# Performance work log

Hardware: AMD Instinct MI355X
Metric: run time of the kernel (lower is better)

## Reference

```python
import jax, jax.numpy as jnp
import numpy as np

B, N, D = 2, 2048, 1024
H, DH = 16, 64
DEPTH = 4
FF = 4
EPS = 1e-3  # keras LayerNormalization default epsilon
SCALE = DH ** -0.5


def setup_inputs() -> dict:
    key = jax.random.key(0)
    ks = jax.random.split(key, 8)
    s = 0.02
    inner = H * DH
    return {
        "x": jax.random.normal(ks[0], (B, N, D), jnp.float32),
        "mask": jnp.ones((B, N), jnp.bool_),
        "ln1_g": jnp.ones((DEPTH, D), jnp.float32),
        "ln1_b": jnp.zeros((DEPTH, D), jnp.float32),
        "Wqkv": jax.random.normal(ks[1], (DEPTH, D, 3 * inner), jnp.float32) * s,
        "Wout": jax.random.normal(ks[2], (DEPTH, inner, D), jnp.float32) * s,
        "bout": jnp.zeros((DEPTH, D), jnp.float32),
        "ln2_g": jnp.ones((DEPTH, D), jnp.float32),
        "ln2_b": jnp.zeros((DEPTH, D), jnp.float32),
        "W1": jax.random.normal(ks[3], (DEPTH, D, 2 * FF * D), jnp.float32) * s,
        "b1": jnp.zeros((DEPTH, 2 * FF * D), jnp.float32),
        "W2": jax.random.normal(ks[4], (DEPTH, FF * D, D), jnp.float32) * s,
        "b2": jnp.zeros((DEPTH, D), jnp.float32),
    }


def _layernorm(x, g, b):
    mu = jnp.mean(x, axis=-1, keepdims=True)
    var = jnp.mean(jnp.square(x - mu), axis=-1, keepdims=True)
    return (x - mu) * jax.lax.rsqrt(var + EPS) * g + b


def _attention(x, mask, Wqkv, Wout, bout):
    b, n, _ = x.shape
    qkv = x @ Wqkv  # [b, n, 3*h*dh]
    q, k, v = jnp.split(qkv, 3, axis=-1)
    split_heads = lambda t: t.reshape(b, n, H, DH).transpose(0, 2, 1, 3)  # b h n d
    q, k, v = split_heads(q), split_heads(k), split_heads(v)
    dots = jnp.einsum("bhid,bhjd->bhij", q, k) * SCALE
    neg = -jnp.finfo(dots.dtype).max
    # padding mask: keep (i valid) & (j valid)
    pm = mask[:, None, :, None] & mask[:, None, None, :]
    dots = jnp.where(pm, dots, neg)
    # causal mask: strict upper triangle masked out (triu with k=1)
    causal = jnp.triu(jnp.ones((n, n), jnp.bool_), k=1)
    dots = jnp.where(causal, neg, dots)
    attn = jax.nn.softmax(dots, axis=-1)
    out = jnp.einsum("bhij,bhjd->bhid", attn, v)
    out = out.transpose(0, 2, 1, 3).reshape(b, n, H * DH)
    return out @ Wout + bout


def _feedforward(x, W1, b1, W2, b2):
    h = x @ W1 + b1
    a, gates = jnp.split(h, 2, axis=-1)
    h = a * jax.nn.gelu(gates, approximate=False)  # GEGLU, tf.nn.gelu exact
    return h @ W2 + b2


def reference(x, mask, ln1_g, ln1_b, Wqkv, Wout, bout, ln2_g, ln2_b, W1, b1, W2, b2):
    for l in range(DEPTH):
        x = x + _attention(_layernorm(x, ln1_g[l], ln1_b[l]), mask, Wqkv[l], Wout[l], bout[l])
        x = x + _feedforward(_layernorm(x, ln2_g[l], ln2_b[l]), W1[l], b1[l], W2[l], b2[l])
    return x
```

## Files before the change

### kernel.cpp

```cpp
#include <hip/hip_runtime.h>


typedef float f32x4 __attribute__((ext_vector_type(4)));
typedef __bf16 bf16x8 __attribute__((ext_vector_type(8)));
typedef unsigned short u16;
typedef unsigned int u32;

#define SCALE2 0.18033688011112042f
#define LN_EPS 1e-3f
#define DEFER_THR 8.0f

__device__ __forceinline__ float fexp2(float x) { return __builtin_amdgcn_exp2f(x); }

__device__ __forceinline__ u16 f2bf(float f) {
  u32 u = __float_as_uint(f);
  u += 0x7fffu + ((u >> 16) & 1u);
  return (u16)(u >> 16);
}

__device__ __forceinline__ void stage16(void* lds_wave_base, const void* gsrc) {
  __builtin_amdgcn_global_load_lds((__attribute__((address_space(1))) void*)gsrc,
                                   (__attribute__((address_space(3))) void*)lds_wave_base,
                                   16, 0, 0);
}

__global__ void wtrans_kernel(const float* __restrict__ W, u16* __restrict__ WT,
                              int K, int N, int permMode) {
  __shared__ float tile[32][33];
  const int n0 = blockIdx.x * 32, k0 = blockIdx.y * 32;
  const float* Wl = W + (size_t)blockIdx.z * K * N;
  u16* WTl = WT + (size_t)blockIdx.z * K * N;
  const int tx = threadIdx.x, ty = threadIdx.y;
#pragma unroll
  for (int i = 0; i < 4; ++i)
    tile[ty + i * 8][tx] = Wl[(size_t)(k0 + ty + i * 8) * N + n0 + tx];
  __syncthreads();
#pragma unroll
  for (int i = 0; i < 4; ++i) {
    const int n = n0 + ty + i * 8;
    int orow;
    if (permMode) {
      orow = (n < 4096) ? (((n >> 4) << 5) + (n & 15))
                        : ((((n - 4096) >> 4) << 5) + 16 + (n & 15));
    } else {
      orow = n;
    }
    WTl[(size_t)orow * K + k0 + tx] = f2bf(tile[tx][ty + i * 8]);
  }
}

__global__ void vtrans_kernel(const u16* __restrict__ qkv, u16* __restrict__ Vt) {
  __shared__ u16 tile[32][33];
  const int t0 = blockIdx.x * 32, d0 = blockIdx.y * 32, bh = blockIdx.z;
  const int b = bh >> 4, h = bh & 15;
  const int tx = threadIdx.x, ty = threadIdx.y;
#pragma unroll
  for (int i = 0; i < 4; ++i)
    tile[ty + i * 8][tx] =
        qkv[((size_t)(b * 2048 + t0 + ty + i * 8)) * 3072 + 2048 + h * 64 + d0 + tx];
  __syncthreads();
#pragma unroll
  for (int i = 0; i < 4; ++i)
    Vt[((size_t)bh * 64 + d0 + ty + i * 8) * 2048 + t0 + tx] = tile[tx][ty + i * 8];
}

__global__ __launch_bounds__(256, 4)
void ln_kernel(const float* __restrict__ x, const float* __restrict__ g,
               const float* __restrict__ b, u16* __restrict__ y) {
  const int row = blockIdx.x, tid = threadIdx.x;
  const float4 v = ((const float4*)(x + (size_t)row * 1024))[tid];
  float s = v.x + v.y + v.z + v.w;
  float s2 = v.x * v.x + v.y * v.y + v.z * v.z + v.w * v.w;
#pragma unroll
  for (int off = 32; off > 0; off >>= 1) {
    s += __shfl_down(s, off);
    s2 += __shfl_down(s2, off);
  }
  __shared__ float ps[8];
  __shared__ float stats[2];
  const int wv = tid >> 6, lane = tid & 63;
  if (lane == 0) { ps[wv] = s; ps[wv + 4] = s2; }
  __syncthreads();
  if (tid == 0) {
    const float S = ps[0] + ps[1] + ps[2] + ps[3];
    const float S2 = ps[4] + ps[5] + ps[6] + ps[7];
    const float mu = S * (1.0f / 1024.0f);
    const float var = S2 * (1.0f / 1024.0f) - mu * mu;
    stats[0] = mu;
    stats[1] = rsqrtf(var + LN_EPS);
  }
  __syncthreads();
  const float mu = stats[0], rs = stats[1];
  const float4 gg = ((const float4*)g)[tid];
  const float4 bb = ((const float4*)b)[tid];
  ushort4 ov;
  ov.x = f2bf((v.x - mu) * rs * gg.x + bb.x);
  ov.y = f2bf((v.y - mu) * rs * gg.y + bb.y);
  ov.z = f2bf((v.z - mu) * rs * gg.z + bb.z);
  ov.w = f2bf((v.w - mu) * rs * gg.w + bb.w);
  ((ushort4*)(y + (size_t)row * 1024))[tid] = ov;
}

template <int EPI, int BM, int BN, int WM, int WN>
__global__ __launch_bounds__(WM * WN * 64, 2)
void gemm2(const u16* __restrict__ A, const u16* __restrict__ B,
           float* __restrict__ resid, const float* __restrict__ bias,
           u16* __restrict__ out, int M, int N, int K) {
  constexpr int NTHR = WM * WN * 64;
  constexpr int MT = BM / WM / 16;
  constexpr int NT = BN / WN / 16;
  constexpr int QM = MT / 4;
  __shared__ __align__(16) u16 lds[2][(BM + BN) * 64];

  const int tid = threadIdx.x;
  const int wv = tid >> 6, lane = tid & 63;
  const int lr = lane & 15, lg = lane >> 4;
  const int wmi = wv / WN, wni = wv % WN;

  const int nwg = (int)(gridDim.x * gridDim.y);
  int id = (int)(blockIdx.y * gridDim.x + blockIdx.x);
  id = (id & 7) * (nwg >> 3) + (id >> 3);
  const int m0 = (id / (int)gridDim.x) * BM, n0 = (id % (int)gridDim.x) * BN;

  auto stage = [&](int bsel, int k0) {
    u16* dstA = &lds[bsel][0];
    u16* dstB = &lds[bsel][BM * 64];
#pragma unroll
    for (int rnd = 0; rnd < (BM * 128) / (NTHR * 16); ++rnd) {
      const int base = rnd * (NTHR * 16) + wv * 1024;
      const int off = base + lane * 16;
      const int row = off >> 7;
      const int k2 = (off & 127) ^ ((row & 7) << 4);
      stage16((char*)dstA + base, A + (size_t)(m0 + row) * K + k0 + (k2 >> 1));
    }
#pragma unroll
    for (int rnd = 0; rnd < (BN * 128) / (NTHR * 16); ++rnd) {
      const int base = rnd * (NTHR * 16) + wv * 1024;
      const int off = base + lane * 16;
      const int row = off >> 7;
      const int k2 = (off & 127) ^ ((row & 7) << 4);
      stage16((char*)dstB + base, B + (size_t)(n0 + row) * K + k0 + (k2 >> 1));
    }
  };

  f32x4 acc[MT][NT] = {};

  const int nT = K >> 6;
  stage(0, 0);
  stage(1, 64);
  asm volatile("s_waitcnt vmcnt(8)\n\ts_barrier" ::: "memory");

  for (int t = 0; t < nT; ++t) {
    const u16* As = &lds[t & 1][0];
    const u16* Bs = &lds[t & 1][BM * 64];
#pragma unroll
    for (int ks = 0; ks < 2; ++ks) {
      bf16x8 bfr[NT];
#pragma unroll
      for (int nt = 0; nt < NT; ++nt) {
        const int row = wni * (BN / WN) + nt * 16 + lr;
        bfr[nt] = *(const bf16x8*)((const char*)Bs + row * 128 +
                                   ((ks * 64 + lg * 16) ^ ((lr & 7) << 4)));
      }
#pragma unroll
      for (int qm = 0; qm < QM; ++qm) {
        bf16x8 afr[4];
#pragma unroll
        for (int i = 0; i < 4; ++i) {
          const int row = wmi * (BM / WM) + (qm * 4 + i) * 16 + lr;
          afr[i] = *(const bf16x8*)((const char*)As + row * 128 +
                                    ((ks * 64 + lg * 16) ^ ((lr & 7) << 4)));
        }
        __builtin_amdgcn_s_setprio(1);
#pragma unroll
        for (int i = 0; i < 4; ++i)
#pragma unroll
          for (int nt = 0; nt < NT; ++nt)
            acc[qm * 4 + i][nt] = __builtin_amdgcn_mfma_f32_16x16x32_bf16(
                afr[i], bfr[nt], acc[qm * 4 + i][nt], 0, 0, 0);
        __builtin_amdgcn_s_setprio(0);
      }
    }
    __syncthreads();
    if (t + 2 < nT) stage(t & 1, (t + 2) * 64);
    asm volatile("s_barrier" ::: "memory");
  }

  const int RB0 = wmi * (BM / WM), CB0 = wni * (BN / WN);
  if (EPI == 0) {
#pragma unroll
    for (int mt = 0; mt < MT; ++mt)
#pragma unroll
      for (int nt = 0; nt < NT; ++nt) {
        const int n = n0 + CB0 + nt * 16 + lr;
#pragma unroll
        for (int r = 0; r < 4; ++r) {
          const int m = m0 + RB0 + mt * 16 + lg * 4 + r;
          out[(size_t)m * N + n] = f2bf(acc[mt][nt][r]);
        }
      }
  } else if (EPI == 1) {
    float bs[NT];
#pragma unroll
    for (int nt = 0; nt < NT; ++nt) bs[nt] = bias[n0 + CB0 + nt * 16 + lr];
#pragma unroll
    for (int mt = 0; mt < MT; ++mt)
#pragma unroll
      for (int nt = 0; nt < NT; ++nt) {
        const int n = n0 + CB0 + nt * 16 + lr;
#pragma unroll
        for (int r = 0; r < 4; ++r) {
          const int m = m0 + RB0 + mt * 16 + lg * 4 + r;
          resid[(size_t)m * N + n] += acc[mt][nt][r] + bs[nt];
        }
      }
  } else {
#pragma unroll
    for (int pt = 0; pt < NT / 2; ++pt) {
      const int colA = ((n0 + CB0 + pt * 32) >> 5) * 16 + lr;
      const float ba = bias[colA];
      const float bg = bias[4096 + colA];
#pragma unroll
      for (int mt = 0; mt < MT; ++mt)
#pragma unroll
        for (int r = 0; r < 4; ++r) {
          const int m = m0 + RB0 + mt * 16 + lg * 4 + r;
          const float a = acc[mt][2 * pt][r] + ba;
          const float g = acc[mt][2 * pt + 1][r] + bg;
          const float gl = 0.5f * g * (1.0f + erff(g * 0.70710678118654752f));
          out[(size_t)m * 4096 + colA] = f2bf(a * gl);
        }
    }
  }
}

__global__ __launch_bounds__(512, 4)
void attn_kernel(const u16* __restrict__ qkv, const u16* __restrict__ Vt,
                 u16* __restrict__ attnout) {
  __shared__ __align__(16) u16 KV[2][2][64 * 64];
  __shared__ __align__(16) u16 Ps[8][16 * 64];

  const int tid = threadIdx.x;
  const int wv = tid >> 6, lane = tid & 63;
  const int lr = lane & 15, lg = lane >> 4;
  const int lin = (int)(blockIdx.y * gridDim.x + blockIdx.x);
  const int xcd = lin & 7, j = lin >> 3;
  const int bh = xcd * 4 + (j >> 4);
  const int pr = j & 15;
  const int b = bh >> 4, h = bh & 15;
  const size_t tokbase = (size_t)b * 2048;
  const int qhi = 31 - pr;
  const int qt = (wv < 4) ? qhi : pr;
  const int ws = wv & 3;
  const int qg = qt * 64 + ws * 16 + lr;

  bf16x8 qf[2];
#pragma unroll
  for (int ks = 0; ks < 2; ++ks)
    qf[ks] = *(const bf16x8*)(qkv + (tokbase + qt * 64 + ws * 16 + lr) * 3072 +
                              h * 64 + ks * 32 + lg * 8);

  f32x4 o[4] = {};
  float m = -1e30f, lp = 0.f;

  const u16* kg_base = qkv + tokbase * 3072 + 1024 + h * 64;
  const u16* vg_base = Vt + (size_t)bh * 64 * 2048;

  const int soff = tid * 16;
  const int srow = soff >> 7;
  const int scol = (soff & 127) ^ ((srow & 7) << 4);
  auto stage = [&](int bsel, int kt2) {
    stage16((char*)&KV[bsel][0][0] + wv * 1024,
            kg_base + (size_t)(kt2 * 64 + srow) * 3072 + (scol >> 1));
    stage16((char*)&KV[bsel][1][0] + wv * 1024,
            vg_base + (size_t)srow * 2048 + kt2 * 64 + (scol >> 1));
  };

  stage(0, 0);
  stage(1, 1);
  asm volatile("s_waitcnt vmcnt(2)\n\ts_barrier" ::: "memory");

  for (int kt = 0; kt <= qhi; ++kt) {
    if (kt <= qt) {
      const char* Ks = (const char*)&KV[kt & 1][0][0];
      const char* Vs = (const char*)&KV[kt & 1][1][0];

      f32x4 s[4] = {};
#pragma unroll
      for (int ks = 0; ks < 2; ++ks)
#pragma unroll
        for (int nt = 0; nt < 4; ++nt) {
          const int row = nt * 16 + lr;
          const bf16x8 kf = *(const bf16x8*)(Ks + row * 128 +
                                             ((ks * 64 + lg * 16) ^ ((lr & 7) << 4)));
          s[nt] = __builtin_amdgcn_mfma_f32_16x16x32_bf16(kf, qf[ks], s[nt], 0, 0, 0);
        }

      float pmax = -1e30f;
      const bool diag = (kt == qt);
#pragma unroll
      for (int nt = 0; nt < 4; ++nt)
#pragma unroll
        for (int r = 0; r < 4; ++r) {
          float v = s[nt][r] * SCALE2;
          if (diag) {
            const int kg = kt * 64 + nt * 16 + lg * 4 + r;
            v = (kg <= qg) ? v : -1e30f;
          }
          s[nt][r] = v;
          pmax = fmaxf(pmax, v);
        }

      if (!__all(pmax - m <= DEFER_THR)) {
        float mx = fmaxf(pmax, __shfl_xor(pmax, 16));
        mx = fmaxf(mx, __shfl_xor(mx, 32));
        const float mn = fmaxf(m, mx);
        const float alpha = fexp2(m - mn);
        m = mn;
        lp *= alpha;
#pragma unroll
        for (int r = 0; r < 4; ++r) {
          const float ar = __shfl(alpha, lg * 4 + r);
#pragma unroll
          for (int dt = 0; dt < 4; ++dt) o[dt][r] *= ar;
        }
      }

#pragma unroll
      for (int nt = 0; nt < 4; ++nt) {
        const float p0 = fexp2(s[nt][0] - m), p1 = fexp2(s[nt][1] - m);
        const float p2 = fexp2(s[nt][2] - m), p3 = fexp2(s[nt][3] - m);
        lp += (p0 + p1) + (p2 + p3);
        uint2 w;
        w.x = (u32)f2bf(p0) | ((u32)f2bf(p1) << 16);
        w.y = (u32)f2bf(p2) | ((u32)f2bf(p3) << 16);
        *(uint2*)((char*)&Ps[wv][0] + lr * 128 + ((nt * 32 + lg * 8) ^ ((lr & 7) << 4))) = w;
      }

      bf16x8 pf[2];
#pragma unroll
      for (int ks = 0; ks < 2; ++ks) {
        const int jp = (ks * 4 + lg) ^ (lr & 7);
        pf[ks] = *(const bf16x8*)(&Ps[wv][0] + lr * 64 + jp * 8);
      }
#pragma unroll
      for (int ks = 0; ks < 2; ++ks)
#pragma unroll
        for (int dt = 0; dt < 4; ++dt) {
          const int row = dt * 16 + lr;
          const bf16x8 vf = *(const bf16x8*)(Vs + row * 128 +
                                             ((ks * 64 + lg * 16) ^ ((lr & 7) << 4)));
          o[dt] = __builtin_amdgcn_mfma_f32_16x16x32_bf16(pf[ks], vf, o[dt], 0, 0, 0);
        }
    }

    __syncthreads();
    if (kt + 2 <= qhi) stage(kt & 1, kt + 2);
    asm volatile("s_barrier" ::: "memory");
  }

  float lsum = lp + __shfl_xor(lp, 16);
  lsum += __shfl_xor(lsum, 32);
#pragma unroll
  for (int r = 0; r < 4; ++r) {
    const float ld = __shfl(lsum, lg * 4 + r);
    const int tok = qt * 64 + ws * 16 + lg * 4 + r;
#pragma unroll
    for (int dt = 0; dt < 4; ++dt)
      attnout[(tokbase + tok) * 1024 + h * 64 + dt * 16 + lr] = f2bf(o[dt][r] / ld);
  }
}

extern "C" void kernel_launch(void* const* d_in, const int* in_sizes, int n_in,
                              void* d_out, int out_size, void* d_ws, size_t ws_size,
                              hipStream_t stream) {
  (void)in_sizes; (void)n_in; (void)ws_size;
  const float* x_in  = (const float*)d_in[0];
  const float* ln1_g = (const float*)d_in[2];
  const float* ln1_b = (const float*)d_in[3];
  const float* Wqkv  = (const float*)d_in[4];
  const float* Wout  = (const float*)d_in[5];
  const float* bout  = (const float*)d_in[6];
  const float* ln2_g = (const float*)d_in[7];
  const float* ln2_b = (const float*)d_in[8];
  const float* W1    = (const float*)d_in[9];
  const float* b1    = (const float*)d_in[10];
  const float* W2    = (const float*)d_in[11];
  const float* b2    = (const float*)d_in[12];
  float* x = (float*)d_out;

  char* ws = (char*)d_ws;
  size_t off = 0;
  auto alloc = [&](size_t bytes) -> void* {
    void* p = ws + off;
    off += (bytes + 255) & ~(size_t)255;
    return p;
  };
  u16* WqkvT = (u16*)alloc(4ull * 3072 * 1024 * 2);
  u16* WoutT = (u16*)alloc(4ull * 1024 * 1024 * 2);
  u16* W1T   = (u16*)alloc(4ull * 8192 * 1024 * 2);
  u16* W2T   = (u16*)alloc(4ull * 1024 * 4096 * 2);
  u16* y     = (u16*)alloc(4096ull * 1024 * 2);
  u16* qkvb  = (u16*)alloc(4096ull * 3072 * 2);
  u16* Vt    = (u16*)alloc(32ull * 64 * 2048 * 2);
  u16* attn  = (u16*)alloc(4096ull * 1024 * 2);
  u16* ff    = (u16*)alloc(4096ull * 4096 * 2);

  hipMemcpyAsync(x, x_in, (size_t)out_size * 4, hipMemcpyDeviceToDevice, stream);

  const dim3 tb(32, 8);
  wtrans_kernel<<<dim3(3072 / 32, 1024 / 32, 4), tb, 0, stream>>>(Wqkv, WqkvT, 1024, 3072, 0);
  wtrans_kernel<<<dim3(1024 / 32, 1024 / 32, 4), tb, 0, stream>>>(Wout, WoutT, 1024, 1024, 0);
  wtrans_kernel<<<dim3(8192 / 32, 1024 / 32, 4), tb, 0, stream>>>(W1, W1T, 1024, 8192, 1);
  wtrans_kernel<<<dim3(1024 / 32, 4096 / 32, 4), tb, 0, stream>>>(W2, W2T, 4096, 1024, 0);

  for (int l = 0; l < 4; ++l) {
    ln_kernel<<<4096, 256, 0, stream>>>(x, ln1_g + l * 1024, ln1_b + l * 1024, y);
    gemm2<0, 128, 128, 2, 2><<<dim3(3072 / 128, 4096 / 128), 256, 0, stream>>>(
        y, WqkvT + (size_t)l * 3072 * 1024, nullptr, nullptr, qkvb, 4096, 3072, 1024);
    vtrans_kernel<<<dim3(64, 2, 32), tb, 0, stream>>>(qkvb, Vt);
    attn_kernel<<<dim3(16, 32), 512, 0, stream>>>(qkvb, Vt, attn);
    gemm2<1, 128, 128, 2, 2><<<dim3(1024 / 128, 4096 / 128), 256, 0, stream>>>(
        attn, WoutT + (size_t)l * 1024 * 1024, x, bout + l * 1024, nullptr, 4096, 1024, 1024);
    ln_kernel<<<4096, 256, 0, stream>>>(x, ln2_g + l * 1024, ln2_b + l * 1024, y);
    gemm2<2, 256, 256, 2, 4><<<dim3(8192 / 256, 4096 / 256), 512, 0, stream>>>(
        y, W1T + (size_t)l * 8192 * 1024, nullptr, b1 + l * 8192, ff, 4096, 8192, 1024);
    gemm2<1, 128, 128, 2, 2><<<dim3(1024 / 128, 4096 / 128), 256, 0, stream>>>(
        ff, W2T + (size_t)l * 1024 * 4096, x, b2 + l * 1024, nullptr, 4096, 1024, 4096);
  }
}
```

Before: 1.163 ms.

## Load full K-tile fragments to registers before issuing next stage and MFMAs

The GEMM main loop now reads all A and B fragments for both k-substeps of the current LDS buffer into registers first, then waits on LDS reads and barriers. It issues the next global-to-LDS prefetch into that same buffer before running all MFMAs, so global loads overlap the MFMA block. The post-MFMA barrier waits on vmcnt so the next buffer is ready. This frees the LDS buffer earlier, at the cost of many more live fragment registers (notably for the 256x256 tile), which may hurt occupancy or cause spills.

Result: no change. 1.162 ms (-0.1%).

```diff
diff --git a/kernel.cpp b/kernel.cpp
--- a/kernel.cpp
+++ b/kernel.cpp
@@ -103,19 +103,19 @@
 
 template <int EPI, int BM, int BN, int WM, int WN>
 __global__ __launch_bounds__(WM * WN * 64, 2)
-void gemm2(const u16* __restrict__ A, const u16* __restrict__ B,
+void gemm3(const u16* __restrict__ A, const u16* __restrict__ B,
            float* __restrict__ resid, const float* __restrict__ bias,
            u16* __restrict__ out, int M, int N, int K) {
   constexpr int NTHR = WM * WN * 64;
   constexpr int MT = BM / WM / 16;
   constexpr int NT = BN / WN / 16;
-  constexpr int QM = MT / 4;
   __shared__ __align__(16) u16 lds[2][(BM + BN) * 64];
 
   const int tid = threadIdx.x;
   const int wv = tid >> 6, lane = tid & 63;
   const int lr = lane & 15, lg = lane >> 4;
   const int wmi = wv / WN, wni = wv % WN;
+  const int RB0 = wmi * (BM / WM), CB0 = wni * (BN / WN);
 
   const int nwg = (int)(gridDim.x * gridDim.y);
   int id = (int)(blockIdx.y * gridDim.x + blockIdx.x);
@@ -151,42 +151,47 @@
   asm volatile("s_waitcnt vmcnt(8)\n\ts_barrier" ::: "memory");
 
   for (int t = 0; t < nT; ++t) {
-    const u16* As = &lds[t & 1][0];
-    const u16* Bs = &lds[t & 1][BM * 64];
+    const char* As = (const char*)&lds[t & 1][0];
+    const char* Bs = (const char*)&lds[t & 1][BM * 64];
+
+    bf16x8 afr[2][MT], bfr[2][NT];
 #pragma unroll
     for (int ks = 0; ks < 2; ++ks) {
-      bf16x8 bfr[NT];
 #pragma unroll
       for (int nt = 0; nt < NT; ++nt) {
-        const int row = wni * (BN / WN) + nt * 16 + lr;
-        bfr[nt] = *(const bf16x8*)((const char*)Bs + row * 128 +
-                                   ((ks * 64 + lg * 16) ^ ((lr & 7) << 4)));
-      }
-#pragma unroll
-      for (int qm = 0; qm < QM; ++qm) {
-        bf16x8 afr[4];
-#pragma unroll
-        for (int i = 0; i < 4; ++i) {
-          const int row = wmi * (BM / WM) + (qm * 4 + i) * 16 + lr;
-          afr[i] = *(const bf16x8*)((const char*)As + row * 128 +
-                                    ((ks * 64 + lg * 16) ^ ((lr & 7) << 4)));
-        }
-        __builtin_amdgcn_s_setprio(1);
-#pragma unroll
-        for (int i = 0; i < 4; ++i)
-#pragma unroll
-          for (int nt = 0; nt < NT; ++nt)
-            acc[qm * 4 + i][nt] = __builtin_amdgcn_mfma_f32_16x16x32_bf16(
-                afr[i], bfr[nt], acc[qm * 4 + i][nt], 0, 0, 0);
-        __builtin_amdgcn_s_setprio(0);
-      }
-    }
-    __syncthreads();
+        const int row = CB0 + nt * 16 + lr;
+        bfr[ks][nt] = *(const bf16x8*)(Bs + row * 128 +
+                                       ((ks * 64 + lg * 16) ^ ((lr & 7) << 4)));
+      }
+#pragma unroll
+      for (int mt = 0; mt < MT; ++mt) {
+        const int row = RB0 + mt * 16 + lr;
+        afr[ks][mt] = *(const bf16x8*)(As + row * 128 +
+                                       ((ks * 64 + lg * 16) ^ ((lr & 7) << 4)));
+      }
+    }
+    __builtin_amdgcn_sched_barrier(0);
+    asm volatile("s_waitcnt lgkmcnt(0)\n\ts_barrier" ::: "memory");
+    __builtin_amdgcn_sched_barrier(0);
     if (t + 2 < nT) stage(t & 1, (t + 2) * 64);
-    asm volatile("s_barrier" ::: "memory");
-  }
-
-  const int RB0 = wmi * (BM / WM), CB0 = wni * (BN / WN);
+    __builtin_amdgcn_s_setprio(1);
+#pragma unroll
+    for (int ks = 0; ks < 2; ++ks)
+#pragma unroll
+      for (int mt = 0; mt < MT; ++mt)
+#pragma unroll
+        for (int nt = 0; nt < NT; ++nt)
+          acc[mt][nt] = __builtin_amdgcn_mfma_f32_16x16x32_bf16(
+              afr[ks][mt], bfr[ks][nt], acc[mt][nt], 0, 0, 0);
+    __builtin_amdgcn_s_setprio(0);
+    if (t + 1 < nT) {
+      if (t + 2 < nT)
+        asm volatile("s_waitcnt vmcnt(8)\n\ts_barrier" ::: "memory");
+      else
+        asm volatile("s_waitcnt vmcnt(0)\n\ts_barrier" ::: "memory");
+    }
+  }
+
   if (EPI == 0) {
 #pragma unroll
     for (int mt = 0; mt < MT; ++mt)
@@ -416,16 +421,16 @@
 
   for (int l = 0; l < 4; ++l) {
     ln_kernel<<<4096, 256, 0, stream>>>(x, ln1_g + l * 1024, ln1_b + l * 1024, y);
-    gemm2<0, 128, 128, 2, 2><<<dim3(3072 / 128, 4096 / 128), 256, 0, stream>>>(
+    gemm3<0, 128, 128, 2, 2><<<dim3(3072 / 128, 4096 / 128), 256, 0, stream>>>(
         y, WqkvT + (size_t)l * 3072 * 1024, nullptr, nullptr, qkvb, 4096, 3072, 1024);
     vtrans_kernel<<<dim3(64, 2, 32), tb, 0, stream>>>(qkvb, Vt);
     attn_kernel<<<dim3(16, 32), 512, 0, stream>>>(qkvb, Vt, attn);
-    gemm2<1, 128, 128, 2, 2><<<dim3(1024 / 128, 4096 / 128), 256, 0, stream>>>(
+    gemm3<1, 128, 128, 2, 2><<<dim3(1024 / 128, 4096 / 128), 256, 0, stream>>>(
         attn, WoutT + (size_t)l * 1024 * 1024, x, bout + l * 1024, nullptr, 4096, 1024, 1024);
     ln_kernel<<<4096, 256, 0, stream>>>(x, ln2_g + l * 1024, ln2_b + l * 1024, y);
-    gemm2<2, 256, 256, 2, 4><<<dim3(8192 / 256, 4096 / 256), 512, 0, stream>>>(
+    gemm3<2, 256, 256, 2, 4><<<dim3(8192 / 256, 4096 / 256), 512, 0, stream>>>(
         y, W1T + (size_t)l * 8192 * 1024, nullptr, b1 + l * 8192, ff, 4096, 8192, 1024);
-    gemm2<1, 128, 128, 2, 2><<<dim3(1024 / 128, 4096 / 128), 256, 0, stream>>>(
+    gemm3<1, 128, 128, 2, 2><<<dim3(1024 / 128, 4096 / 128), 256, 0, stream>>>(
         ff, W2T + (size_t)l * 1024 * 4096, x, b2 + l * 1024, nullptr, 4096, 1024, 4096);
   }
 }
```
